# Kernel optimization log

Measured on AMD Instinct MI355X. Metric: run time of the kernel, lower is better.

The kernel has to match this reference:

```python
import jax, jax.numpy as jnp
import numpy as np
from jax import lax

T = 262144
H = 64
OUT = 16  # 2**MEMORY_LENGTH with MEMORY_LENGTH=4


def setup_inputs() -> dict:
    key = jax.random.key(0)
    ks = jax.random.split(key, 11)
    s = 0.1  # keep gates out of saturation
    return {
        "y": jax.random.normal(ks[0], (T, 1), jnp.float32),
        "W_ih0": s * jax.random.normal(ks[1], (4 * H, 1), jnp.float32),
        "W_hh0": s * jax.random.normal(ks[2], (4 * H, H), jnp.float32),
        "b_ih0": s * jax.random.normal(ks[3], (4 * H,), jnp.float32),
        "b_hh0": s * jax.random.normal(ks[4], (4 * H,), jnp.float32),
        "W_ih1": s * jax.random.normal(ks[5], (4 * H, H), jnp.float32),
        "W_hh1": s * jax.random.normal(ks[6], (4 * H, H), jnp.float32),
        "b_ih1": s * jax.random.normal(ks[7], (4 * H,), jnp.float32),
        "b_hh1": s * jax.random.normal(ks[8], (4 * H,), jnp.float32),
        "W_lin": s * jax.random.normal(ks[9], (OUT, H), jnp.float32),
        "b_lin": s * jax.random.normal(ks[10], (OUT,), jnp.float32),
    }


def _lstm_layer(x, W_ih, W_hh, b_ih, b_hh):
    # x: [T, in]. PyTorch gate order: i, f, g, o. Zero initial state.
    h = W_hh.shape[1]
    xp = x @ W_ih.T + (b_ih + b_hh)  # precompute input contribution: [T, 4H]

    def step(carry, xt):
        h_t, c_t = carry
        gates = xt + h_t @ W_hh.T
        i, f, g, o = jnp.split(gates, 4)
        i = jax.nn.sigmoid(i)
        f = jax.nn.sigmoid(f)
        g = jnp.tanh(g)
        o = jax.nn.sigmoid(o)
        c_new = f * c_t + i * g
        h_new = o * jnp.tanh(c_new)
        return (h_new, c_new), h_new

    init = (jnp.zeros((h,), x.dtype), jnp.zeros((h,), x.dtype))
    _, hs = lax.scan(step, init, xp)
    return hs  # [T, H]


def reference(y, W_ih0, W_hh0, b_ih0, b_hh0, W_ih1, W_hh1, b_ih1, b_hh1, W_lin, b_lin):
    # phase == 'train' branch of RNNDetector.forward
    h1 = _lstm_layer(y, W_ih0, W_hh0, b_ih0, b_hh0)   # [T, 64]
    h2 = _lstm_layer(h1, W_ih1, W_hh1, b_ih1, b_hh1)  # [T, 64]
    return h2 @ W_lin.T + b_lin                        # [T, 16]
```

## Files before the change

### kernel.cpp

```cpp
#include <hip/hip_runtime.h>


constexpr int T  = 262144;
constexpr int B  = 32;
constexpr int NB = T / B;
constexpr int RS = 2 * B;
constexpr int K_SS = NB + 3;

typedef _Float16 h2v __attribute__((ext_vector_type(2)));
typedef unsigned u4 __attribute__((ext_vector_type(4)));
typedef float    f4 __attribute__((ext_vector_type(4)));

__device__ __forceinline__ float rcp_f(float x) { return __builtin_amdgcn_rcpf(x); }

#define BARRIER() asm volatile("s_waitcnt lgkmcnt(0)\n\ts_barrier" ::: "memory")

static __device__ __forceinline__ float fd(unsigned w, unsigned h, float acc) {
#if __has_builtin(__builtin_amdgcn_fdot2)
  return __builtin_amdgcn_fdot2(__builtin_bit_cast(h2v, w),
                                __builtin_bit_cast(h2v, h), acc, false);
#else
  h2v a = __builtin_bit_cast(h2v, w), b = __builtin_bit_cast(h2v, h);
  acc = fmaf((float)a.x, (float)b.x, acc);
  acc = fmaf((float)a.y, (float)b.y, acc);
  return acc;
#endif
}

#define DP4(acc, W, H) { acc = fd((W).x, (H).x, acc); acc = fd((W).y, (H).y, acc); \
                         acc = fd((W).z, (H).z, acc); acc = fd((W).w, (H).w, acc); }

#define DPPX1(x) __builtin_bit_cast(float, __builtin_amdgcn_mov_dpp(            \
                    __builtin_bit_cast(int, (x)), 0xB1, 0xF, 0xF, true))
#define DPPX2(x) __builtin_bit_cast(float, __builtin_amdgcn_mov_dpp(            \
                    __builtin_bit_cast(int, (x)), 0x4E, 0xF, 0xF, true))

__device__ __forceinline__ float exp2_f(float x) {
  float r; asm("v_exp_f32 %0, %1" : "=v"(r) : "v"(x)); return r;
}
__device__ __forceinline__ float exp2n_g(float u) {
  return exp2_f(fminf(-u, 126.f));
}
__device__ __forceinline__ float sig_u(float u) {
  return rcp_f(1.f + exp2n_g(u));
}
__device__ __forceinline__ float tanh_u(float u) {
  float e2 = exp2n_g(u);
  return (1.f - e2) * rcp_f(1.f + e2);
}
__device__ __forceinline__ float tanh_c(float c) {
  return tanh_u(c * 2.8853900817779268f);
}

constexpr float L2E  = 1.4426950408889634f;
constexpr float L2E2 = 2.8853900817779268f;

__device__ unsigned f16rne(float f) {
  unsigned u = __float_as_uint(f);
  unsigned s = (u >> 16) & 0x8000u;
  int e = (int)((u >> 23) & 0xff) - 127;
  unsigned m = u & 0x7fffffu;
  if (e < -14) return s;
  unsigned h = s | (unsigned)((e + 15) << 10) | (m >> 13);
  unsigned rem = m & 0x1fffu;
  h += (rem > 0x1000u) || (rem == 0x1000u && (h & 1u));
  return h;
}

__global__ void pack_w(const float* __restrict__ Whh0,
                       const float* __restrict__ Whh1,
                       const float* __restrict__ Wih1,
                       const float* __restrict__ Wlin,
                       unsigned* __restrict__ ws) {
  int i = blockIdx.x * 256 + threadIdx.x;
  if (i >= 25088) return;
  float v0, v1, sc = 1.f;
  if (i < 24576) {
    int w = i >> 13, rem = i & 8191, l = rem >> 7, d = rem & 127;
    int r = d >> 5, kp = d & 31, row = r * 64 + l;
    const float* src = (w == 0) ? Whh0 : (w == 1) ? Whh1 : Wih1;
    v0 = src[row * 64 + 2 * kp]; v1 = src[row * 64 + 2 * kp + 1];
    sc = (r == 2) ? L2E2 : L2E;
  } else {
    int j = i - 24576, l = j >> 3, d = j & 7;
    int m = l >> 2, kq = l & 3, k = kq * 16 + 2 * d;
    v0 = Wlin[m * 64 + k]; v1 = Wlin[m * 64 + k + 1];
  }
  ws[i] = f16rne(v0 * sc) | (f16rne(v1 * sc) << 16);
}

#define DECLW32(wp)                                                            \
  u4 W0=(wp)[0],  W1=(wp)[1],  W2=(wp)[2],  W3=(wp)[3],                        \
     W4=(wp)[4],  W5=(wp)[5],  W6=(wp)[6],  W7=(wp)[7],                        \
     W8=(wp)[8],  W9=(wp)[9],  W10=(wp)[10],W11=(wp)[11],                      \
     W12=(wp)[12],W13=(wp)[13],W14=(wp)[14],W15=(wp)[15],                      \
     W16=(wp)[16],W17=(wp)[17],W18=(wp)[18],W19=(wp)[19],                      \
     W20=(wp)[20],W21=(wp)[21],W22=(wp)[22],W23=(wp)[23],                      \
     W24=(wp)[24],W25=(wp)[25],W26=(wp)[26],W27=(wp)[27],                      \
     W28=(wp)[28],W29=(wp)[29],W30=(wp)[30],W31=(wp)[31]

#define PINW8(a,b,c,d,e,f,g,h)                                                 \
  asm volatile("" : "+v"(a), "+v"(b), "+v"(c), "+v"(d),                        \
                    "+v"(e), "+v"(f), "+v"(g), "+v"(h))
#define PINALL() { PINW8(W0,W1,W2,W3,W4,W5,W6,W7);                             \
                   PINW8(W8,W9,W10,W11,W12,W13,W14,W15);                       \
                   PINW8(W16,W17,W18,W19,W20,W21,W22,W23);                     \
                   PINW8(W24,W25,W26,W27,W28,W29,W30,W31); }

__global__ __launch_bounds__(192)
__attribute__((amdgpu_waves_per_eu(1, 1)))
void rnn_fused(
    const float* __restrict__ y,
    const float* __restrict__ Wih0, const float* __restrict__ bih0,
    const float* __restrict__ bhh0,
    const float* __restrict__ bih1, const float* __restrict__ bhh1,
    const float* __restrict__ blin,
    const unsigned* __restrict__ ws,
    float* __restrict__ out)
{
  const int tid = threadIdx.x;
  __shared__ __align__(16) unsigned h0r[RS * 32];
  __shared__ __align__(16) unsigned h1r[RS * 32];
  __shared__ __align__(16) float    xpf[RS * 256];

  for (int j = tid; j < RS * 32; j += 192) { h0r[j] = 0u; h1r[j] = 0u; }
  __syncthreads();

  if (tid < 64) {
    __builtin_amdgcn_s_setprio(1);
    const int e = tid;
    const u4* wp = (const u4*)(ws + e * 128);
    DECLW32(wp);
    float bbi = (bih0[e] + bhh0[e]) * L2E;
    float bbf = (bih0[64 + e] + bhh0[64 + e]) * L2E;
    float bbg = (bih0[128 + e] + bhh0[128 + e]) * L2E2;
    float bbo = (bih0[192 + e] + bhh0[192 + e]) * L2E;
    float wii = Wih0[e] * L2E, wif = Wih0[64 + e] * L2E;
    float wig = Wih0[128 + e] * L2E2, wio = Wih0[192 + e] * L2E;
    float c0 = 0.f;
    float ylv = y[e & (B - 1)];
    _Float16* h0h = (_Float16*)h0r;

    for (int k = 0; k < K_SS; ++k) {
      if (k < NB) {
        float yln = (k + 1 < NB) ? y[(k + 1) * B + (e & (B - 1))] : 0.f;
        const int base = k * B;
        #pragma unroll 1
        for (int i = 0; i < B; ++i) {
          const int s = base + i;
          PINALL();
          float ys = __builtin_bit_cast(float,
              __builtin_amdgcn_readlane(__builtin_bit_cast(int, ylv), i));
          const u4* hp = (const u4*)(h0r + ((s - 1) & (RS - 1)) * 32);
          u4 H0=hp[0],H1=hp[1],H2=hp[2],H3=hp[3],H4=hp[4],H5=hp[5],H6=hp[6],H7=hp[7];
          float ai0=0,ai1=0, af0=0,af1=0, ag0=0,ag1=0, ao0=0,ao1=0;
          DP4(ai0,W0,H0)  DP4(af0,W8,H0)  DP4(ag0,W16,H0) DP4(ao0,W24,H0)
          DP4(ai1,W1,H1)  DP4(af1,W9,H1)  DP4(ag1,W17,H1) DP4(ao1,W25,H1)
          DP4(ai0,W2,H2)  DP4(af0,W10,H2) DP4(ag0,W18,H2) DP4(ao0,W26,H2)
          DP4(ai1,W3,H3)  DP4(af1,W11,H3) DP4(ag1,W19,H3) DP4(ao1,W27,H3)
          DP4(ai0,W4,H4)  DP4(af0,W12,H4) DP4(ag0,W20,H4) DP4(ao0,W28,H4)
          DP4(ai1,W5,H5)  DP4(af1,W13,H5) DP4(ag1,W21,H5) DP4(ao1,W29,H5)
          DP4(ai0,W6,H6)  DP4(af0,W14,H6) DP4(ag0,W22,H6) DP4(ao0,W30,H6)
          DP4(ai1,W7,H7)  DP4(af1,W15,H7) DP4(ag1,W23,H7) DP4(ao1,W31,H7)
          float I = sig_u((ai0 + ai1) + fmaf(ys, wii, bbi));
          float F = sig_u((af0 + af1) + fmaf(ys, wif, bbf));
          float G = tanh_u((ag0 + ag1) + fmaf(ys, wig, bbg));
          float O = sig_u((ao0 + ao1) + fmaf(ys, wio, bbo));
          c0 = fmaf(F, c0, I * G);
          float h = O * tanh_c(c0);
          h0h[(s & (RS - 1)) * 64 + e] = (_Float16)h;
        }
        ylv = yln;
      }
      BARRIER();
    }
  } else if (tid < 128) {
    const int e = tid - 64;
    const u4* wp = (const u4*)(ws + 16384 + e * 128);
    DECLW32(wp);
    const u4* hwp = (const u4*)(ws + 24576 + e * 8);
    u4 HW0 = hwp[0], HW1 = hwp[1];
    float bb0 = (bih1[e] + bhh1[e]) * L2E;
    float bb1 = (bih1[64 + e] + bhh1[64 + e]) * L2E;
    float bb2 = (bih1[128 + e] + bhh1[128 + e]) * L2E2;
    float bb3 = (bih1[192 + e] + bhh1[192 + e]) * L2E;
    const int m = e >> 2, kq = e & 3;
    float bl = (kq == 0) ? blin[m] : 0.f;

    for (int k = 0; k < K_SS; ++k) {
      if (k >= 1 && k <= NB) {
        const int base = (k - 1) * B;
        #pragma unroll 1
        for (int i = 0; i < B; ++i) {
          const int t = base + i;
          const int slot = t & (RS - 1);
          PINALL();
          const u4* hp = (const u4*)(h0r + slot * 32);
          u4 H0=hp[0],H1=hp[1],H2=hp[2],H3=hp[3],H4=hp[4],H5=hp[5],H6=hp[6],H7=hp[7];
          float p0a=0,p0b=0, p1a=0,p1b=0, p2a=0,p2b=0, p3a=0,p3b=0;
          DP4(p0a,W0,H0) DP4(p1a,W8,H0)  DP4(p2a,W16,H0) DP4(p3a,W24,H0)
          DP4(p0b,W1,H1) DP4(p1b,W9,H1)  DP4(p2b,W17,H1) DP4(p3b,W25,H1)
          DP4(p0a,W2,H2) DP4(p1a,W10,H2) DP4(p2a,W18,H2) DP4(p3a,W26,H2)
          DP4(p0b,W3,H3) DP4(p1b,W11,H3) DP4(p2b,W19,H3) DP4(p3b,W27,H3)
          DP4(p0a,W4,H4) DP4(p1a,W12,H4) DP4(p2a,W20,H4) DP4(p3a,W28,H4)
          DP4(p0b,W5,H5) DP4(p1b,W13,H5) DP4(p2b,W21,H5) DP4(p3b,W29,H5)
          DP4(p0a,W6,H6) DP4(p1a,W14,H6) DP4(p2a,W22,H6) DP4(p3a,W30,H6)
          DP4(p0b,W7,H7) DP4(p1b,W15,H7) DP4(p2b,W23,H7) DP4(p3b,W31,H7)
          f4 v;
          v.x = (p0a + p0b) + bb0;
          v.y = (p1a + p1b) + bb1;
          v.z = (p2a + p2b) + bb2;
          v.w = (p3a + p3b) + bb3;
          *(f4*)(xpf + slot * 256 + e * 4) = v;
        }
      }
      if (k >= 3) {
        const int base = (k - 3) * B;
        #pragma unroll 1
        for (int i = 0; i < B; ++i) {
          const int t = base + i;
          const int slot = t & (RS - 1);
          const u4* h1p = (const u4*)(h1r + slot * 32 + kq * 8);
          u4 X0 = h1p[0], X1 = h1p[1];
          float r2 = 0.f;
          DP4(r2, HW0, X0) DP4(r2, HW1, X1)
          r2 += DPPX1(r2);
          r2 += DPPX2(r2);
          if (kq == 0) out[t * 16 + m] = r2 + bl;
        }
      }
      BARRIER();
    }
  } else {
    __builtin_amdgcn_s_setprio(1);
    const int e = tid - 128;
    const u4* wp = (const u4*)(ws + 8192 + e * 128);
    DECLW32(wp);
    float c1 = 0.f;
    _Float16* h1h = (_Float16*)h1r;

    for (int k = 0; k < K_SS; ++k) {
      if (k >= 2 && k <= NB + 1) {
        const int base = (k - 2) * B;
        #pragma unroll 1
        for (int i = 0; i < B; ++i) {
          const int t = base + i;
          const int slot = t & (RS - 1);
          PINALL();
          const f4 xq = *(const f4*)(xpf + slot * 256 + e * 4);
          const u4* hp = (const u4*)(h1r + ((t - 1) & (RS - 1)) * 32);
          u4 H0=hp[0],H1=hp[1],H2=hp[2],H3=hp[3],H4=hp[4],H5=hp[5],H6=hp[6],H7=hp[7];
          float ai0=0,ai1=0, af0=0,af1=0, ag0=0,ag1=0, ao0=0,ao1=0;
          DP4(ai0,W0,H0)  DP4(af0,W8,H0)  DP4(ag0,W16,H0) DP4(ao0,W24,H0)
          DP4(ai1,W1,H1)  DP4(af1,W9,H1)  DP4(ag1,W17,H1) DP4(ao1,W25,H1)
          DP4(ai0,W2,H2)  DP4(af0,W10,H2) DP4(ag0,W18,H2) DP4(ao0,W26,H2)
          DP4(ai1,W3,H3)  DP4(af1,W11,H3) DP4(ag1,W19,H3) DP4(ao1,W27,H3)
          DP4(ai0,W4,H4)  DP4(af0,W12,H4) DP4(ag0,W20,H4) DP4(ao0,W28,H4)
          DP4(ai1,W5,H5)  DP4(af1,W13,H5) DP4(ag1,W21,H5) DP4(ao1,W29,H5)
          DP4(ai0,W6,H6)  DP4(af0,W14,H6) DP4(ag0,W22,H6) DP4(ao0,W30,H6)
          DP4(ai1,W7,H7)  DP4(af1,W15,H7) DP4(ag1,W23,H7) DP4(ao1,W31,H7)
          float I = sig_u(xq.x + (ai0 + ai1));
          float F = sig_u(xq.y + (af0 + af1));
          float G = tanh_u(xq.z + (ag0 + ag1));
          float O = sig_u(xq.w + (ao0 + ao1));
          c1 = fmaf(F, c1, I * G);
          float h = O * tanh_c(c1);
          h1h[slot * 64 + e] = (_Float16)h;
        }
      }
      BARRIER();
    }
  }
}

extern "C" void kernel_launch(void* const* d_in, const int* in_sizes, int n_in,
                              void* d_out, int out_size, void* d_ws, size_t ws_size,
                              hipStream_t stream) {
  const float* y    = (const float*)d_in[0];
  const float* Wih0 = (const float*)d_in[1];
  const float* Whh0 = (const float*)d_in[2];
  const float* bih0 = (const float*)d_in[3];
  const float* bhh0 = (const float*)d_in[4];
  const float* Wih1 = (const float*)d_in[5];
  const float* Whh1 = (const float*)d_in[6];
  const float* bih1 = (const float*)d_in[7];
  const float* bhh1 = (const float*)d_in[8];
  const float* Wlin = (const float*)d_in[9];
  const float* blin = (const float*)d_in[10];
  unsigned* ws = (unsigned*)d_ws;

  pack_w<<<dim3(98), dim3(256), 0, stream>>>(Whh0, Whh1, Wih1, Wlin, ws);
  rnn_fused<<<dim3(1), dim3(192), 0, stream>>>(
      y, Wih0, bih0, bhh0, bih1, bhh1, blin, ws, (float*)d_out);
}
```

Measured before the change: 114.8 ms.

## Merge layer-0 and layer-1 recurrences into one wave with interleaved steps

The two LSTM recurrences, previously on separate waves, now run in a single wave that holds both weight sets in registers and interleaves one layer-0 step with one layer-1 step per iteration, which cuts the block to two waves. The aim is to use instruction-level parallelism between the two independent dependency chains inside one wave instead of relying on the wave scheduler. The pre-activation scale is also folded in as a negative, so the sigmoid drops its negate and clamp. This doubles the weight register footprint in that wave and risks spills, and each step now serialises both layers' arithmetic in one instruction stream.

```diff
diff --git a/kernel.cpp b/kernel.cpp
--- a/kernel.cpp
+++ b/kernel.cpp
@@ -10,6 +10,9 @@
 typedef _Float16 h2v __attribute__((ext_vector_type(2)));
 typedef unsigned u4 __attribute__((ext_vector_type(4)));
 typedef float    f4 __attribute__((ext_vector_type(4)));
+
+struct TT { static constexpr bool value = true; };
+struct FF { static constexpr bool value = false; };
 
 __device__ __forceinline__ float rcp_f(float x) { return __builtin_amdgcn_rcpf(x); }
 
@@ -38,18 +41,15 @@
 __device__ __forceinline__ float exp2_f(float x) {
   float r; asm("v_exp_f32 %0, %1" : "=v"(r) : "v"(x)); return r;
 }
-__device__ __forceinline__ float exp2n_g(float u) {
-  return exp2_f(fminf(-u, 126.f));
-}
-__device__ __forceinline__ float sig_u(float u) {
-  return rcp_f(1.f + exp2n_g(u));
-}
-__device__ __forceinline__ float tanh_u(float u) {
-  float e2 = exp2n_g(u);
+__device__ __forceinline__ float sig_n(float un) {
+  return rcp_f(1.f + exp2_f(un));
+}
+__device__ __forceinline__ float tanh_n(float un) {
+  float e2 = exp2_f(fminf(un, 126.f));
   return (1.f - e2) * rcp_f(1.f + e2);
 }
-__device__ __forceinline__ float tanh_c(float c) {
-  return tanh_u(c * 2.8853900817779268f);
+__device__ __forceinline__ float tanh_cn(float c) {
+  return tanh_n(c * -2.8853900817779268f);
 }
 
 constexpr float L2E  = 1.4426950408889634f;
@@ -80,7 +80,7 @@
     int r = d >> 5, kp = d & 31, row = r * 64 + l;
     const float* src = (w == 0) ? Whh0 : (w == 1) ? Whh1 : Wih1;
     v0 = src[row * 64 + 2 * kp]; v1 = src[row * 64 + 2 * kp + 1];
-    sc = (r == 2) ? L2E2 : L2E;
+    sc = (r == 2) ? -L2E2 : -L2E;
   } else {
     int j = i - 24576, l = j >> 3, d = j & 7;
     int m = l >> 2, kq = l & 3, k = kq * 16 + 2 * d;
@@ -99,15 +99,29 @@
      W24=(wp)[24],W25=(wp)[25],W26=(wp)[26],W27=(wp)[27],                      \
      W28=(wp)[28],W29=(wp)[29],W30=(wp)[30],W31=(wp)[31]
 
+#define DECLX32(wp)                                                            \
+  u4 X0=(wp)[0],  X1=(wp)[1],  X2=(wp)[2],  X3=(wp)[3],                        \
+     X4=(wp)[4],  X5=(wp)[5],  X6=(wp)[6],  X7=(wp)[7],                        \
+     X8=(wp)[8],  X9=(wp)[9],  X10=(wp)[10],X11=(wp)[11],                      \
+     X12=(wp)[12],X13=(wp)[13],X14=(wp)[14],X15=(wp)[15],                      \
+     X16=(wp)[16],X17=(wp)[17],X18=(wp)[18],X19=(wp)[19],                      \
+     X20=(wp)[20],X21=(wp)[21],X22=(wp)[22],X23=(wp)[23],                      \
+     X24=(wp)[24],X25=(wp)[25],X26=(wp)[26],X27=(wp)[27],                      \
+     X28=(wp)[28],X29=(wp)[29],X30=(wp)[30],X31=(wp)[31]
+
 #define PINW8(a,b,c,d,e,f,g,h)                                                 \
   asm volatile("" : "+v"(a), "+v"(b), "+v"(c), "+v"(d),                        \
                     "+v"(e), "+v"(f), "+v"(g), "+v"(h))
-#define PINALL() { PINW8(W0,W1,W2,W3,W4,W5,W6,W7);                             \
-                   PINW8(W8,W9,W10,W11,W12,W13,W14,W15);                       \
-                   PINW8(W16,W17,W18,W19,W20,W21,W22,W23);                     \
-                   PINW8(W24,W25,W26,W27,W28,W29,W30,W31); }
-
-__global__ __launch_bounds__(192)
+#define PINALLW() { PINW8(W0,W1,W2,W3,W4,W5,W6,W7);                            \
+                    PINW8(W8,W9,W10,W11,W12,W13,W14,W15);                      \
+                    PINW8(W16,W17,W18,W19,W20,W21,W22,W23);                    \
+                    PINW8(W24,W25,W26,W27,W28,W29,W30,W31); }
+#define PINALLX() { PINW8(X0,X1,X2,X3,X4,X5,X6,X7);                            \
+                    PINW8(X8,X9,X10,X11,X12,X13,X14,X15);                      \
+                    PINW8(X16,X17,X18,X19,X20,X21,X22,X23);                    \
+                    PINW8(X24,X25,X26,X27,X28,X29,X30,X31); }
+
+__global__ __launch_bounds__(128)
 __attribute__((amdgpu_waves_per_eu(1, 1)))
 void rnn_fused(
     const float* __restrict__ y,
@@ -123,32 +137,35 @@
   __shared__ __align__(16) unsigned h1r[RS * 32];
   __shared__ __align__(16) float    xpf[RS * 256];
 
-  for (int j = tid; j < RS * 32; j += 192) { h0r[j] = 0u; h1r[j] = 0u; }
+  for (int j = tid; j < RS * 32; j += 128) { h0r[j] = 0u; h1r[j] = 0u; }
   __syncthreads();
 
   if (tid < 64) {
     __builtin_amdgcn_s_setprio(1);
     const int e = tid;
-    const u4* wp = (const u4*)(ws + e * 128);
-    DECLW32(wp);
-    float bbi = (bih0[e] + bhh0[e]) * L2E;
-    float bbf = (bih0[64 + e] + bhh0[64 + e]) * L2E;
-    float bbg = (bih0[128 + e] + bhh0[128 + e]) * L2E2;
-    float bbo = (bih0[192 + e] + bhh0[192 + e]) * L2E;
-    float wii = Wih0[e] * L2E, wif = Wih0[64 + e] * L2E;
-    float wig = Wih0[128 + e] * L2E2, wio = Wih0[192 + e] * L2E;
-    float c0 = 0.f;
+    const u4* wpA = (const u4*)(ws + e * 128);
+    const u4* wpB = (const u4*)(ws + 8192 + e * 128);
+    DECLW32(wpA);
+    DECLX32(wpB);
+    float bbi = -(bih0[e] + bhh0[e]) * L2E;
+    float bbf = -(bih0[64 + e] + bhh0[64 + e]) * L2E;
+    float bbg = -(bih0[128 + e] + bhh0[128 + e]) * L2E2;
+    float bbo = -(bih0[192 + e] + bhh0[192 + e]) * L2E;
+    float wii = -Wih0[e] * L2E, wif = -Wih0[64 + e] * L2E;
+    float wig = -Wih0[128 + e] * L2E2, wio = -Wih0[192 + e] * L2E;
+    float c0 = 0.f, c1 = 0.f;
     float ylv = y[e & (B - 1)];
     _Float16* h0h = (_Float16*)h0r;
-
-    for (int k = 0; k < K_SS; ++k) {
-      if (k < NB) {
-        float yln = (k + 1 < NB) ? y[(k + 1) * B + (e & (B - 1))] : 0.f;
-        const int base = k * B;
-        #pragma unroll 1
-        for (int i = 0; i < B; ++i) {
-          const int s = base + i;
-          PINALL();
+    _Float16* h1h = (_Float16*)h1r;
+
+    auto blk = [&](auto L0C, auto L1C, int k) {
+      constexpr bool DL0 = decltype(L0C)::value;
+      constexpr bool DL1 = decltype(L1C)::value;
+      #pragma unroll 1
+      for (int i = 0; i < B; ++i) {
+        PINALLW(); PINALLX();
+        if constexpr (DL0) {
+          const int s = k * B + i;
           float ys = __builtin_bit_cast(float,
               __builtin_amdgcn_readlane(__builtin_bit_cast(int, ylv), i));
           const u4* hp = (const u4*)(h0r + ((s - 1) & (RS - 1)) * 32);
@@ -162,28 +179,60 @@
           DP4(ai1,W5,H5)  DP4(af1,W13,H5) DP4(ag1,W21,H5) DP4(ao1,W29,H5)
           DP4(ai0,W6,H6)  DP4(af0,W14,H6) DP4(ag0,W22,H6) DP4(ao0,W30,H6)
           DP4(ai1,W7,H7)  DP4(af1,W15,H7) DP4(ag1,W23,H7) DP4(ao1,W31,H7)
-          float I = sig_u((ai0 + ai1) + fmaf(ys, wii, bbi));
-          float F = sig_u((af0 + af1) + fmaf(ys, wif, bbf));
-          float G = tanh_u((ag0 + ag1) + fmaf(ys, wig, bbg));
-          float O = sig_u((ao0 + ao1) + fmaf(ys, wio, bbo));
-          c0 = fmaf(F, c0, I * G);
-          float h = O * tanh_c(c0);
+          float I = sig_n((ai0 + ai1) + fmaf(ys, wii, bbi));
+          float F = sig_n((af0 + af1) + fmaf(ys, wif, bbf));
+          float Gg = tanh_n((ag0 + ag1) + fmaf(ys, wig, bbg));
+          float O = sig_n((ao0 + ao1) + fmaf(ys, wio, bbo));
+          c0 = fmaf(F, c0, I * Gg);
+          float h = O * tanh_cn(c0);
           h0h[(s & (RS - 1)) * 64 + e] = (_Float16)h;
         }
-        ylv = yln;
+        if constexpr (DL1) {
+          const int t = k * B + i - 2 * B;
+          const int slot = t & (RS - 1);
+          const f4 xq = *(const f4*)(xpf + slot * 256 + e * 4);
+          const u4* jp = (const u4*)(h1r + ((t - 1) & (RS - 1)) * 32);
+          u4 J0=jp[0],J1=jp[1],J2=jp[2],J3=jp[3],J4=jp[4],J5=jp[5],J6=jp[6],J7=jp[7];
+          float bi0=0,bi1=0, bf0=0,bf1=0, bg0=0,bg1=0, bo0=0,bo1=0;
+          DP4(bi0,X0,J0)  DP4(bf0,X8,J0)  DP4(bg0,X16,J0) DP4(bo0,X24,J0)
+          DP4(bi1,X1,J1)  DP4(bf1,X9,J1)  DP4(bg1,X17,J1) DP4(bo1,X25,J1)
+          DP4(bi0,X2,J2)  DP4(bf0,X10,J2) DP4(bg0,X18,J2) DP4(bo0,X26,J2)
+          DP4(bi1,X3,J3)  DP4(bf1,X11,J3) DP4(bg1,X19,J3) DP4(bo1,X27,J3)
+          DP4(bi0,X4,J4)  DP4(bf0,X12,J4) DP4(bg0,X20,J4) DP4(bo0,X28,J4)
+          DP4(bi1,X5,J5)  DP4(bf1,X13,J5) DP4(bg1,X21,J5) DP4(bo1,X29,J5)
+          DP4(bi0,X6,J6)  DP4(bf0,X14,J6) DP4(bg0,X22,J6) DP4(bo0,X30,J6)
+          DP4(bi1,X7,J7)  DP4(bf1,X15,J7) DP4(bg1,X23,J7) DP4(bo1,X31,J7)
+          float I = sig_n(xq.x + (bi0 + bi1));
+          float F = sig_n(xq.y + (bf0 + bf1));
+          float Gg = tanh_n(xq.z + (bg0 + bg1));
+          float O = sig_n(xq.w + (bo0 + bo1));
+          c1 = fmaf(F, c1, I * Gg);
+          float h = O * tanh_cn(c1);
+          h1h[slot * 64 + e] = (_Float16)h;
+        }
       }
+    };
+
+    for (int k = 0; k < K_SS; ++k) {
+      const bool l0 = (k < NB);
+      const bool l1 = (k >= 2 && k <= NB + 1);
+      float yln = (l0 && k + 1 < NB) ? y[(k + 1) * B + (e & (B - 1))] : 0.f;
+      if (l0 && l1)      blk(TT{}, TT{}, k);
+      else if (l0)       blk(TT{}, FF{}, k);
+      else if (l1)       blk(FF{}, TT{}, k);
+      ylv = yln;
       BARRIER();
     }
-  } else if (tid < 128) {
+  } else {
     const int e = tid - 64;
     const u4* wp = (const u4*)(ws + 16384 + e * 128);
     DECLW32(wp);
     const u4* hwp = (const u4*)(ws + 24576 + e * 8);
     u4 HW0 = hwp[0], HW1 = hwp[1];
-    float bb0 = (bih1[e] + bhh1[e]) * L2E;
-    float bb1 = (bih1[64 + e] + bhh1[64 + e]) * L2E;
-    float bb2 = (bih1[128 + e] + bhh1[128 + e]) * L2E2;
-    float bb3 = (bih1[192 + e] + bhh1[192 + e]) * L2E;
+    float bb0 = -(bih1[e] + bhh1[e]) * L2E;
+    float bb1 = -(bih1[64 + e] + bhh1[64 + e]) * L2E;
+    float bb2 = -(bih1[128 + e] + bhh1[128 + e]) * L2E2;
+    float bb3 = -(bih1[192 + e] + bhh1[192 + e]) * L2E;
     const int m = e >> 2, kq = e & 3;
     float bl = (kq == 0) ? blin[m] : 0.f;
 
@@ -194,7 +243,7 @@
         for (int i = 0; i < B; ++i) {
           const int t = base + i;
           const int slot = t & (RS - 1);
-          PINALL();
+          PINALLW();
           const u4* hp = (const u4*)(h0r + slot * 32);
           u4 H0=hp[0],H1=hp[1],H2=hp[2],H3=hp[3],H4=hp[4],H5=hp[5],H6=hp[6],H7=hp[7];
           float p0a=0,p0b=0, p1a=0,p1b=0, p2a=0,p2b=0, p3a=0,p3b=0;
@@ -221,51 +270,12 @@
           const int t = base + i;
           const int slot = t & (RS - 1);
           const u4* h1p = (const u4*)(h1r + slot * 32 + kq * 8);
-          u4 X0 = h1p[0], X1 = h1p[1];
+          u4 Y0 = h1p[0], Y1 = h1p[1];
           float r2 = 0.f;
-          DP4(r2, HW0, X0) DP4(r2, HW1, X1)
+          DP4(r2, HW0, Y0) DP4(r2, HW1, Y1)
           r2 += DPPX1(r2);
           r2 += DPPX2(r2);
           if (kq == 0) out[t * 16 + m] = r2 + bl;
-        }
-      }
-      BARRIER();
-    }
-  } else {
-    __builtin_amdgcn_s_setprio(1);
-    const int e = tid - 128;
-    const u4* wp = (const u4*)(ws + 8192 + e * 128);
-    DECLW32(wp);
-    float c1 = 0.f;
-    _Float16* h1h = (_Float16*)h1r;
-
-    for (int k = 0; k < K_SS; ++k) {
-      if (k >= 2 && k <= NB + 1) {
-        const int base = (k - 2) * B;
-        #pragma unroll 1
-        for (int i = 0; i < B; ++i) {
-          const int t = base + i;
-          const int slot = t & (RS - 1);
-          PINALL();
-          const f4 xq = *(const f4*)(xpf + slot * 256 + e * 4);
-          const u4* hp = (const u4*)(h1r + ((t - 1) & (RS - 1)) * 32);
-          u4 H0=hp[0],H1=hp[1],H2=hp[2],H3=hp[3],H4=hp[4],H5=hp[5],H6=hp[6],H7=hp[7];
-          float ai0=0,ai1=0, af0=0,af1=0, ag0=0,ag1=0, ao0=0,ao1=0;
-          DP4(ai0,W0,H0)  DP4(af0,W8,H0)  DP4(ag0,W16,H0) DP4(ao0,W24,H0)
-          DP4(ai1,W1,H1)  DP4(af1,W9,H1)  DP4(ag1,W17,H1) DP4(ao1,W25,H1)
-          DP4(ai0,W2,H2)  DP4(af0,W10,H2) DP4(ag0,W18,H2) DP4(ao0,W26,H2)
-          DP4(ai1,W3,H3)  DP4(af1,W11,H3) DP4(ag1,W19,H3) DP4(ao1,W27,H3)
-          DP4(ai0,W4,H4)  DP4(af0,W12,H4) DP4(ag0,W20,H4) DP4(ao0,W28,H4)
-          DP4(ai1,W5,H5)  DP4(af1,W13,H5) DP4(ag1,W21,H5) DP4(ao1,W29,H5)
-          DP4(ai0,W6,H6)  DP4(af0,W14,H6) DP4(ag0,W22,H6) DP4(ao0,W30,H6)
-          DP4(ai1,W7,H7)  DP4(af1,W15,H7) DP4(ag1,W23,H7) DP4(ao1,W31,H7)
-          float I = sig_u(xq.x + (ai0 + ai1));
-          float F = sig_u(xq.y + (af0 + af1));
-          float G = tanh_u(xq.z + (ag0 + ag1));
-          float O = sig_u(xq.w + (ao0 + ao1));
-          c1 = fmaf(F, c1, I * G);
-          float h = O * tanh_c(c1);
-          h1h[slot * 64 + e] = (_Float16)h;
         }
       }
       BARRIER();
@@ -290,6 +300,6 @@
   unsigned* ws = (unsigned*)d_ws;
 
   pack_w<<<dim3(98), dim3(256), 0, stream>>>(Whh0, Whh1, Wih1, Wlin, ws);
-  rnn_fused<<<dim3(1), dim3(192), 0, stream>>>(
+  rnn_fused<<<dim3(1), dim3(128), 0, stream>>>(
       y, Wih0, bih0, bhh0, bih1, bhh1, blin, ws, (float*)d_out);
 }
```

After: 339.6 ms. +195.9%, slower.

## Replace per-lane fdot2 gate matvecs with MFMA 16x16x32 f16 instructions

Applied to the files above, without the earlier changes.

The three 64x256 recurrent and input matvecs per step now run on MFMA 16x16x32 f16 instructions instead of per-lane fdot2 loops. The h vector is broadcast as the A operand and the weights are repacked into B-fragment layout. Each lane picks its gate result from the MFMA outputs with lane-group selects. The xp staging buffer is re-laid out with padding to match the new ownership. Most of each MFMA tile is wasted because the batch is one row, and MFMA latency on the serial recurrence path may exceed the dot-product chain it replaces.

```diff
diff --git a/kernel.cpp b/kernel.cpp
--- a/kernel.cpp
+++ b/kernel.cpp
@@ -7,9 +7,10 @@
 constexpr int RS = 2 * B;
 constexpr int K_SS = NB + 3;
 
-typedef _Float16 h2v __attribute__((ext_vector_type(2)));
-typedef unsigned u4 __attribute__((ext_vector_type(4)));
-typedef float    f4 __attribute__((ext_vector_type(4)));
+typedef _Float16 h2v  __attribute__((ext_vector_type(2)));
+typedef _Float16 f16x8 __attribute__((ext_vector_type(8)));
+typedef unsigned u4   __attribute__((ext_vector_type(4)));
+typedef float    f4   __attribute__((ext_vector_type(4)));
 
 __device__ __forceinline__ float rcp_f(float x) { return __builtin_amdgcn_rcpf(x); }
 
@@ -26,9 +27,20 @@
   return acc;
 #endif
 }
-
 #define DP4(acc, W, H) { acc = fd((W).x, (H).x, acc); acc = fd((W).y, (H).y, acc); \
                          acc = fd((W).z, (H).z, acc); acc = fd((W).w, (H).w, acc); }
+
+__device__ __forceinline__ f4 mf(u4 a, u4 b, f4 c) {
+  return __builtin_amdgcn_mfma_f32_16x16x32_f16(
+      __builtin_bit_cast(f16x8, a), __builtin_bit_cast(f16x8, b), c, 0, 0, 0);
+}
+
+__device__ __forceinline__ float sel4(float x0, float x1, float x2, float x3,
+                                      bool b0, bool b1) {
+  float lo = b0 ? x1 : x0;
+  float hi = b0 ? x3 : x2;
+  return b1 ? hi : lo;
+}
 
 #define DPPX1(x) __builtin_bit_cast(float, __builtin_amdgcn_mov_dpp(            \
                     __builtin_bit_cast(int, (x)), 0xB1, 0xF, 0xF, true))
@@ -41,9 +53,7 @@
 __device__ __forceinline__ float exp2n_g(float u) {
   return exp2_f(fminf(-u, 126.f));
 }
-__device__ __forceinline__ float sig_u(float u) {
-  return rcp_f(1.f + exp2n_g(u));
-}
+__device__ __forceinline__ float sig_u(float u)  { return rcp_f(1.f + exp2n_g(u)); }
 __device__ __forceinline__ float tanh_u(float u) {
   float e2 = exp2n_g(u);
   return (1.f - e2) * rcp_f(1.f + e2);
@@ -77,10 +87,13 @@
   float v0, v1, sc = 1.f;
   if (i < 24576) {
     int w = i >> 13, rem = i & 8191, l = rem >> 7, d = rem & 127;
-    int r = d >> 5, kp = d & 31, row = r * 64 + l;
+    int n = d >> 3, s = (d >> 2) & 1, q = d & 3;
+    int c = l & 15, g = l >> 4;
+    int row = n * 16 + c;
+    int col = s * 32 + 8 * g + 2 * q;
     const float* src = (w == 0) ? Whh0 : (w == 1) ? Whh1 : Wih1;
-    v0 = src[row * 64 + 2 * kp]; v1 = src[row * 64 + 2 * kp + 1];
-    sc = (r == 2) ? L2E2 : L2E;
+    v0 = src[row * 64 + col]; v1 = src[row * 64 + col + 1];
+    sc = ((n >> 2) == 2) ? L2E2 : L2E;
   } else {
     int j = i - 24576, l = j >> 3, d = j & 7;
     int m = l >> 2, kq = l & 3, k = kq * 16 + 2 * d;
@@ -106,6 +119,24 @@
                    PINW8(W8,W9,W10,W11,W12,W13,W14,W15);                       \
                    PINW8(W16,W17,W18,W19,W20,W21,W22,W23);                     \
                    PINW8(W24,W25,W26,W27,W28,W29,W30,W31); }
+
+#define MFMA16(A0u, A1u)                                                       \
+  f4 a0  = mf(A0u, W0,  Z4); a0  = mf(A1u, W1,  a0);                           \
+  f4 a1  = mf(A0u, W2,  Z4); a1  = mf(A1u, W3,  a1);                           \
+  f4 a2  = mf(A0u, W4,  Z4); a2  = mf(A1u, W5,  a2);                           \
+  f4 a3  = mf(A0u, W6,  Z4); a3  = mf(A1u, W7,  a3);                           \
+  f4 a4  = mf(A0u, W8,  Z4); a4  = mf(A1u, W9,  a4);                           \
+  f4 a5  = mf(A0u, W10, Z4); a5  = mf(A1u, W11, a5);                           \
+  f4 a6  = mf(A0u, W12, Z4); a6  = mf(A1u, W13, a6);                           \
+  f4 a7  = mf(A0u, W14, Z4); a7  = mf(A1u, W15, a7);                           \
+  f4 a8  = mf(A0u, W16, Z4); a8  = mf(A1u, W17, a8);                           \
+  f4 a9  = mf(A0u, W18, Z4); a9  = mf(A1u, W19, a9);                           \
+  f4 a10 = mf(A0u, W20, Z4); a10 = mf(A1u, W21, a10);                          \
+  f4 a11 = mf(A0u, W22, Z4); a11 = mf(A1u, W23, a11);                          \
+  f4 a12 = mf(A0u, W24, Z4); a12 = mf(A1u, W25, a12);                          \
+  f4 a13 = mf(A0u, W26, Z4); a13 = mf(A1u, W27, a13);                          \
+  f4 a14 = mf(A0u, W28, Z4); a14 = mf(A1u, W29, a14);                          \
+  f4 a15 = mf(A0u, W30, Z4); a15 = mf(A1u, W31, a15);
 
 __global__ __launch_bounds__(192)
 __attribute__((amdgpu_waves_per_eu(1, 1)))
@@ -121,14 +152,17 @@
   const int tid = threadIdx.x;
   __shared__ __align__(16) unsigned h0r[RS * 32];
   __shared__ __align__(16) unsigned h1r[RS * 32];
-  __shared__ __align__(16) float    xpf[RS * 256];
+  __shared__ __align__(16) float    xpf[RS * 320];
 
   for (int j = tid; j < RS * 32; j += 192) { h0r[j] = 0u; h1r[j] = 0u; }
   __syncthreads();
 
+  const f4 Z4 = {0.f, 0.f, 0.f, 0.f};
+
   if (tid < 64) {
     __builtin_amdgcn_s_setprio(1);
-    const int e = tid;
+    const int e = tid, g = e >> 4;
+    const bool b0 = (g & 1) != 0, b1 = (g & 2) != 0;
     const u4* wp = (const u4*)(ws + e * 128);
     DECLW32(wp);
     float bbi = (bih0[e] + bhh0[e]) * L2E;
@@ -151,21 +185,17 @@
           PINALL();
           float ys = __builtin_bit_cast(float,
               __builtin_amdgcn_readlane(__builtin_bit_cast(int, ylv), i));
-          const u4* hp = (const u4*)(h0r + ((s - 1) & (RS - 1)) * 32);
-          u4 H0=hp[0],H1=hp[1],H2=hp[2],H3=hp[3],H4=hp[4],H5=hp[5],H6=hp[6],H7=hp[7];
-          float ai0=0,ai1=0, af0=0,af1=0, ag0=0,ag1=0, ao0=0,ao1=0;
-          DP4(ai0,W0,H0)  DP4(af0,W8,H0)  DP4(ag0,W16,H0) DP4(ao0,W24,H0)
-          DP4(ai1,W1,H1)  DP4(af1,W9,H1)  DP4(ag1,W17,H1) DP4(ao1,W25,H1)
-          DP4(ai0,W2,H2)  DP4(af0,W10,H2) DP4(ag0,W18,H2) DP4(ao0,W26,H2)
-          DP4(ai1,W3,H3)  DP4(af1,W11,H3) DP4(ag1,W19,H3) DP4(ao1,W27,H3)
-          DP4(ai0,W4,H4)  DP4(af0,W12,H4) DP4(ag0,W20,H4) DP4(ao0,W28,H4)
-          DP4(ai1,W5,H5)  DP4(af1,W13,H5) DP4(ag1,W21,H5) DP4(ao1,W29,H5)
-          DP4(ai0,W6,H6)  DP4(af0,W14,H6) DP4(ag0,W22,H6) DP4(ao0,W30,H6)
-          DP4(ai1,W7,H7)  DP4(af1,W15,H7) DP4(ag1,W23,H7) DP4(ao1,W31,H7)
-          float I = sig_u((ai0 + ai1) + fmaf(ys, wii, bbi));
-          float F = sig_u((af0 + af1) + fmaf(ys, wif, bbf));
-          float G = tanh_u((ag0 + ag1) + fmaf(ys, wig, bbg));
-          float O = sig_u((ao0 + ao1) + fmaf(ys, wio, bbo));
+          const u4* ap = (const u4*)(h0r + ((s - 1) & (RS - 1)) * 32);
+          u4 A0u = ap[g], A1u = ap[4 + g];
+          MFMA16(A0u, A1u)
+          float ti = sel4(a0[0],  a1[0],  a2[0],  a3[0],  b0, b1);
+          float tf = sel4(a4[0],  a5[0],  a6[0],  a7[0],  b0, b1);
+          float tg = sel4(a8[0],  a9[0],  a10[0], a11[0], b0, b1);
+          float to = sel4(a12[0], a13[0], a14[0], a15[0], b0, b1);
+          float I = sig_u(ti + fmaf(ys, wii, bbi));
+          float F = sig_u(tf + fmaf(ys, wif, bbf));
+          float G = tanh_u(tg + fmaf(ys, wig, bbg));
+          float O = sig_u(to + fmaf(ys, wio, bbo));
           c0 = fmaf(F, c0, I * G);
           float h = O * tanh_c(c0);
           h0h[(s & (RS - 1)) * 64 + e] = (_Float16)h;
@@ -175,15 +205,23 @@
       BARRIER();
     }
   } else if (tid < 128) {
-    const int e = tid - 64;
+    const int e = tid - 64, g = e >> 4, c = e & 15;
+    const bool b0 = (g & 1) != 0, b1 = (g & 2) != 0;
     const u4* wp = (const u4*)(ws + 16384 + e * 128);
     DECLW32(wp);
     const u4* hwp = (const u4*)(ws + 24576 + e * 8);
     u4 HW0 = hwp[0], HW1 = hwp[1];
-    float bb0 = (bih1[e] + bhh1[e]) * L2E;
-    float bb1 = (bih1[64 + e] + bhh1[64 + e]) * L2E;
-    float bb2 = (bih1[128 + e] + bhh1[128 + e]) * L2E2;
-    float bb3 = (bih1[192 + e] + bhh1[192 + e]) * L2E;
+    float bbx, bby, bbz, bbw;
+    {
+      int R0 = (4 * g + 0) * 16 + c, R1 = (4 * g + 1) * 16 + c;
+      int R2 = (4 * g + 2) * 16 + c, R3 = (4 * g + 3) * 16 + c;
+      float s0 = (((4 * g + 0) >> 2) == 2) ? L2E2 : L2E;
+      float s1 = (((4 * g + 1) >> 2) == 2) ? L2E2 : L2E;
+      float s2 = (((4 * g + 2) >> 2) == 2) ? L2E2 : L2E;
+      float s3 = (((4 * g + 3) >> 2) == 2) ? L2E2 : L2E;
+      bbx = (bih1[R0] + bhh1[R0]) * s0; bby = (bih1[R1] + bhh1[R1]) * s1;
+      bbz = (bih1[R2] + bhh1[R2]) * s2; bbw = (bih1[R3] + bhh1[R3]) * s3;
+    }
     const int m = e >> 2, kq = e & 3;
     float bl = (kq == 0) ? blin[m] : 0.f;
 
@@ -195,23 +233,15 @@
           const int t = base + i;
           const int slot = t & (RS - 1);
           PINALL();
-          const u4* hp = (const u4*)(h0r + slot * 32);
-          u4 H0=hp[0],H1=hp[1],H2=hp[2],H3=hp[3],H4=hp[4],H5=hp[5],H6=hp[6],H7=hp[7];
-          float p0a=0,p0b=0, p1a=0,p1b=0, p2a=0,p2b=0, p3a=0,p3b=0;
-          DP4(p0a,W0,H0) DP4(p1a,W8,H0)  DP4(p2a,W16,H0) DP4(p3a,W24,H0)
-          DP4(p0b,W1,H1) DP4(p1b,W9,H1)  DP4(p2b,W17,H1) DP4(p3b,W25,H1)
-          DP4(p0a,W2,H2) DP4(p1a,W10,H2) DP4(p2a,W18,H2) DP4(p3a,W26,H2)
-          DP4(p0b,W3,H3) DP4(p1b,W11,H3) DP4(p2b,W19,H3) DP4(p3b,W27,H3)
-          DP4(p0a,W4,H4) DP4(p1a,W12,H4) DP4(p2a,W20,H4) DP4(p3a,W28,H4)
-          DP4(p0b,W5,H5) DP4(p1b,W13,H5) DP4(p2b,W21,H5) DP4(p3b,W29,H5)
-          DP4(p0a,W6,H6) DP4(p1a,W14,H6) DP4(p2a,W22,H6) DP4(p3a,W30,H6)
-          DP4(p0b,W7,H7) DP4(p1b,W15,H7) DP4(p2b,W23,H7) DP4(p3b,W31,H7)
-          f4 v;
-          v.x = (p0a + p0b) + bb0;
-          v.y = (p1a + p1b) + bb1;
-          v.z = (p2a + p2b) + bb2;
-          v.w = (p3a + p3b) + bb3;
-          *(f4*)(xpf + slot * 256 + e * 4) = v;
+          const u4* ap = (const u4*)(h0r + slot * 32);
+          u4 A0u = ap[g], A1u = ap[4 + g];
+          MFMA16(A0u, A1u)
+          float vx = sel4(a0[0], a4[0], a8[0],  a12[0], b0, b1) + bbx;
+          float vy = sel4(a1[0], a5[0], a9[0],  a13[0], b0, b1) + bby;
+          float vz = sel4(a2[0], a6[0], a10[0], a14[0], b0, b1) + bbz;
+          float vw = sel4(a3[0], a7[0], a11[0], a15[0], b0, b1) + bbw;
+          f4 v = {vx, vy, vz, vw};
+          *(f4*)(xpf + slot * 320 + c * 20 + 4 * g) = v;
         }
       }
       if (k >= 3) {
@@ -233,7 +263,8 @@
     }
   } else {
     __builtin_amdgcn_s_setprio(1);
-    const int e = tid - 128;
+    const int e = tid - 128, g = e >> 4, c = e & 15;
+    const bool b0 = (g & 1) != 0, b1 = (g & 2) != 0;
     const u4* wp = (const u4*)(ws + 8192 + e * 128);
     DECLW32(wp);
     float c1 = 0.f;
@@ -247,22 +278,19 @@
           const int t = base + i;
           const int slot = t & (RS - 1);
           PINALL();
-          const f4 xq = *(const f4*)(xpf + slot * 256 + e * 4);
-          const u4* hp = (const u4*)(h1r + ((t - 1) & (RS - 1)) * 32);
-          u4 H0=hp[0],H1=hp[1],H2=hp[2],H3=hp[3],H4=hp[4],H5=hp[5],H6=hp[6],H7=hp[7];
-          float ai0=0,ai1=0, af0=0,af1=0, ag0=0,ag1=0, ao0=0,ao1=0;
-          DP4(ai0,W0,H0)  DP4(af0,W8,H0)  DP4(ag0,W16,H0) DP4(ao0,W24,H0)
-          DP4(ai1,W1,H1)  DP4(af1,W9,H1)  DP4(ag1,W17,H1) DP4(ao1,W25,H1)
-          DP4(ai0,W2,H2)  DP4(af0,W10,H2) DP4(ag0,W18,H2) DP4(ao0,W26,H2)
-          DP4(ai1,W3,H3)  DP4(af1,W11,H3) DP4(ag1,W19,H3) DP4(ao1,W27,H3)
-          DP4(ai0,W4,H4)  DP4(af0,W12,H4) DP4(ag0,W20,H4) DP4(ao0,W28,H4)
-          DP4(ai1,W5,H5)  DP4(af1,W13,H5) DP4(ag1,W21,H5) DP4(ao1,W29,H5)
-          DP4(ai0,W6,H6)  DP4(af0,W14,H6) DP4(ag0,W22,H6) DP4(ao0,W30,H6)
-          DP4(ai1,W7,H7)  DP4(af1,W15,H7) DP4(ag1,W23,H7) DP4(ao1,W31,H7)
-          float I = sig_u(xq.x + (ai0 + ai1));
-          float F = sig_u(xq.y + (af0 + af1));
-          float G = tanh_u(xq.z + (ag0 + ag1));
-          float O = sig_u(xq.w + (ao0 + ao1));
+          const float* xb = xpf + slot * 320 + c * 20;
+          float xi = xb[g], xf = xb[4 + g], xg2 = xb[8 + g], xo = xb[12 + g];
+          const u4* ap = (const u4*)(h1r + ((t - 1) & (RS - 1)) * 32);
+          u4 A0u = ap[g], A1u = ap[4 + g];
+          MFMA16(A0u, A1u)
+          float ti = sel4(a0[0],  a1[0],  a2[0],  a3[0],  b0, b1);
+          float tf = sel4(a4[0],  a5[0],  a6[0],  a7[0],  b0, b1);
+          float tg = sel4(a8[0],  a9[0],  a10[0], a11[0], b0, b1);
+          float to = sel4(a12[0], a13[0], a14[0], a15[0], b0, b1);
+          float I = sig_u(ti + xi);
+          float F = sig_u(tf + xf);
+          float G = tanh_u(tg + xg2);
+          float O = sig_u(to + xo);
           c1 = fmaf(F, c1, I * G);
           float h = O * tanh_c(c1);
           h1h[slot * 64 + e] = (_Float16)h;
```

Measured after the change: 113.3 ms. About the same (-1.3%).
